# Kernel tuning notes

Hardware: AMD Instinct MI355X
Metric: run time of the kernel (lower is better)

The kernel has to match this reference:

```python
import jax, jax.numpy as jnp
import numpy as np

B = 2048      # batch (number of event graphs)
NU = 128      # nodes in 'upstream' star graph per sample
ND = 128      # nodes in 'downstream' star graph per sample
FEAT = 10     # raw feature columns; fp[:, :7] used, column -3 (=7) is split flag
IN_DIM = 7    # state_dim + 1 + 2
HID = 64      # hidden1
TAU = 22      # tau_num
ALPHA = 0.2


def star_adj(n):
    # prepare_eg: edges[0,:]=1, symmetrized, diagonal zeroed -> star graph around node 0
    idx = jnp.arange(n)
    return (((idx[:, None] == 0) | (idx[None, :] == 0)) & (idx[:, None] != idx[None, :])).astype(jnp.float32)


def gat(h, W, a, adj, concat):
    # pyGAT GraphAttentionLayer (dropout=0): h [B,n,f], W [f,d], a [2d,1]
    d = W.shape[1]
    Wh = jnp.einsum('bnf,fd->bnd', h, W)                      # [B,n,d]
    e = Wh @ a[:d] + jnp.swapaxes(Wh @ a[d:], 1, 2)           # [B,n,n]
    e = jax.nn.leaky_relu(e, ALPHA)
    e = jnp.where(adj > 0, e, -9e15)
    att = jax.nn.softmax(e, axis=-1)
    hp = jnp.einsum('bnm,bmd->bnd', att, Wh)                  # [B,n,d]
    return jax.nn.elu(hp) if concat else hp


def setup_inputs() -> dict:
    key = jax.random.key(0)
    ks = jax.random.split(key, 12)
    fp = jax.random.normal(ks[0], (B, NU + ND, FEAT), dtype=jnp.float32)
    # column -3: first NU rows negative (u side), last ND rows positive (d side)
    fp = fp.at[:, :NU, FEAT - 3].set(-1.0)
    fp = fp.at[:, NU:, FEAT - 3].set(1.0)
    s = 0.1
    return {
        'fp': fp,
        'u_att_W': jax.random.normal(ks[1], (IN_DIM, HID), jnp.float32) * s,
        'u_att_a': jax.random.normal(ks[2], (2 * HID, 1), jnp.float32) * s,
        'u_out_W': jax.random.normal(ks[3], (HID, HID), jnp.float32) * s,
        'u_out_a': jax.random.normal(ks[4], (2 * HID, 1), jnp.float32) * s,
        'd_att_W': jax.random.normal(ks[5], (IN_DIM, HID), jnp.float32) * s,
        'd_att_a': jax.random.normal(ks[6], (2 * HID, 1), jnp.float32) * s,
        'd_out_W': jax.random.normal(ks[7], (HID, HID), jnp.float32) * s,
        'd_out_a': jax.random.normal(ks[8], (2 * HID, 1), jnp.float32) * s,
        'fc2_W': jax.random.normal(ks[9], (HID, TAU), jnp.float32) * s,
        'fc2_b': jax.random.normal(ks[10], (TAU,), jnp.float32) * s,
    }


def reference(fp, u_att_W, u_att_a, u_out_W, u_out_a,
              d_att_W, d_att_a, d_out_W, d_out_a, fc2_W, fc2_b):
    # static split by the sign of column -3 (fp is constructed so the first NU
    # rows have flag<=0 and the last ND rows have flag>=0, matching prepare_eg)
    u_x = fp[:, :NU, :IN_DIM]   # [B,NU,7]
    d_x = fp[:, NU:, :IN_DIM]   # [B,ND,7]
    u_adj = star_adj(NU)
    d_adj = star_adj(ND)
    # u_egat: 1 attention head (concat->elu) then out layer (no elu), sum over nodes
    u_h = gat(gat(u_x, u_att_W, u_att_a, u_adj, True), u_out_W, u_out_a, u_adj, False)
    u_g = jnp.sum(u_h, axis=1)  # [B,HID]
    d_h = gat(gat(d_x, d_att_W, d_att_a, d_adj, True), d_out_W, d_out_a, d_adj, False)
    d_g = jnp.sum(d_h, axis=1)  # [B,HID]
    a = jax.nn.relu((u_g + d_g) @ fc2_W + fc2_b)  # [B,TAU]
    # torch.sort result is discarded; forward returns W.clamp(0, 10)
    return jnp.clip(a, 0.0, 10.0)
```

## Files before the change

### kernel.cpp

```cpp
#include <hip/hip_runtime.h>
#include <math.h>

#define NB     2048
#define FEAT   10
#define IN_DIM 7
#define HID    64
#define TAU    22
#define ALPHA  0.2f

__global__ __launch_bounds__(256) void gat_star_one(
    const float* __restrict__ fp,
    const float* __restrict__ uW1, const float* __restrict__ uA1,
    const float* __restrict__ uW2,
    const float* __restrict__ dW1, const float* __restrict__ dA1,
    const float* __restrict__ dW2,
    const float* __restrict__ fcW, const float* __restrict__ fcB,
    float* __restrict__ out)
{
    __shared__ float vv[2][2][HID];
    __shared__ float pt[2][2][HID];

    const int tid  = threadIdx.x;
    const int wave = tid >> 6;
    const int lane = tid & 63;
    const int it   = wave >> 1;
    const int half = wave & 1;
    const int item = blockIdx.x * 2 + it;

    const float* xbase = fp + (size_t)item * 256 * FEAT + half * 128 * FEAT;
    const float* pAp = xbase + lane * FEAT;
    const float* pBp = pAp + 64 * FEAT;
    const float2 a0 = *(const float2*)(pAp + 0);
    const float2 a1 = *(const float2*)(pAp + 2);
    const float2 a2 = *(const float2*)(pAp + 4);
    const float  a6 = pAp[6];
    const float2 b0 = *(const float2*)(pBp + 0);
    const float2 b1 = *(const float2*)(pBp + 2);
    const float2 b2 = *(const float2*)(pBp + 4);
    const float  b6 = pBp[6];

    const float* W1 = half ? dW1 : uW1;
    const float* A1 = half ? dA1 : uA1;
    float w1c[IN_DIM];
    #pragma unroll
    for (int f = 0; f < IN_DIM; ++f) w1c[f] = W1[f * HID + lane];
    const float alo = A1[lane];
    const float ahi = A1[HID + lane];

    float sv1[IN_DIM], sv2[IN_DIM];
    #pragma unroll
    for (int f = 0; f < IN_DIM; ++f) {
        float p1 = w1c[f] * alo;
        float p2 = w1c[f] * ahi;
        #pragma unroll
        for (int o = 32; o; o >>= 1) {
            p1 += __shfl_xor(p1, o);
            p2 += __shfl_xor(p2, o);
        }
        sv1[f] = p1; sv2[f] = p2;
    }

    float xA[IN_DIM], xB[IN_DIM];
    xA[0] = a0.x; xA[1] = a0.y; xA[2] = a1.x; xA[3] = a1.y;
    xA[4] = a2.x; xA[5] = a2.y; xA[6] = a6;
    xB[0] = b0.x; xB[1] = b0.y; xB[2] = b1.x; xB[3] = b1.y;
    xB[4] = b2.x; xB[5] = b2.y; xB[6] = b6;

    float x0[IN_DIM];
    #pragma unroll
    for (int f = 0; f < IN_DIM; ++f) x0[f] = __shfl(xA[f], 0);

    float s1 = 0.f, sA = 0.f, sB = 0.f;
    #pragma unroll
    for (int f = 0; f < IN_DIM; ++f) {
        s1 = fmaf(x0[f], sv1[f], s1);
        sA = fmaf(xA[f], sv2[f], sA);
        sB = fmaf(xB[f], sv2[f], sB);
    }
    float eA = s1 + sA; eA = (eA >= 0.f) ? eA : ALPHA * eA;
    float eB = s1 + sB; eB = (eB >= 0.f) ? eB : ALPHA * eB;

    const float qA = (lane == 0) ? 0.f : __expf(eA);
    const float qB = __expf(eB);
    float c[8];
    #pragma unroll
    for (int f = 0; f < IN_DIM; ++f) c[f] = fmaf(qA, xA[f], qB * xB[f]);
    c[7] = qA + qB;
    #pragma unroll
    for (int o = 32; o; o >>= 1) {
        #pragma unroll
        for (int j = 0; j < 8; ++j) c[j] += __shfl_xor(c[j], o);
    }
    const float inv = 1.0f / c[7];

    float h0 = 0.f, h1 = 0.f;
    #pragma unroll
    for (int f = 0; f < IN_DIM; ++f) {
        h0 = fmaf(c[f],  w1c[f], h0);
        h1 = fmaf(x0[f], w1c[f], h1);
    }
    h0 *= inv;
    h0 = (h0 > 0.f) ? h0 : (__expf(h0) - 1.f);
    h1 = (h1 > 0.f) ? h1 : (__expf(h1) - 1.f);
    vv[it][half][lane] = h1 + 127.f * h0;
    __syncthreads();

    {
        const float* W2 = half ? dW2 : uW2;
        const float* v  = vv[it][half];
        float s = 0.f;
        #pragma unroll 16
        for (int k = 0; k < HID; ++k) s = fmaf(v[k], W2[k * HID + lane], s);
        pt[it][half][lane] = s;
    }
    __syncthreads();

    if (half == 0) {
        const float* p0 = pt[it][0];
        const float* p1 = pt[it][1];
        int t = lane & 31; if (t > TAU - 1) t = TAU - 1;
        const int jb = (lane >> 5) << 5;
        float s = 0.f;
        #pragma unroll 8
        for (int jj = 0; jj < 32; ++jj) {
            const int j = jb + jj;
            s = fmaf(p0[j] + p1[j], fcW[j * TAU + t], s);
        }
        s += __shfl_xor(s, 32);
        if (lane < TAU) {
            s += fcB[lane];
            s = fminf(fmaxf(s, 0.f), 10.f);
            out[(size_t)item * TAU + lane] = s;
        }
    }
}

extern "C" void kernel_launch(void* const* d_in, const int* in_sizes, int n_in,
                              void* d_out, int out_size, void* d_ws, size_t ws_size,
                              hipStream_t stream) {
    const float* fp  = (const float*)d_in[0];
    const float* uW1 = (const float*)d_in[1];
    const float* uA1 = (const float*)d_in[2];
    const float* uW2 = (const float*)d_in[3];
    const float* dW1 = (const float*)d_in[5];
    const float* dA1 = (const float*)d_in[6];
    const float* dW2 = (const float*)d_in[7];
    const float* fcW = (const float*)d_in[9];
    const float* fcB = (const float*)d_in[10];
    float* out = (float*)d_out;

    gat_star_one<<<NB / 2, 256, 0, stream>>>(fp, uW1, uA1, uW2,
                                             dW1, dA1, dW2, fcW, fcB, out);
}
```

Baseline: 14.99 us.

## Use DPP wave reductions, per-wave fc2 partials, and wave barriers instead of block syncs

Replaces the shuffle-based butterfly reductions with DPP row/bank operations plus a readlane. The 14 attention-vector dot products are now computed per lane into LDS instead of by cross-lane reductions. Node 0's features are read directly from memory rather than broadcast by shuffle. Each wave computes its own partial fc2 product and only one block-wide sync remains before the final combine, with multiple accumulators added to break FMA dependency chains. The aim is to cut cross-lane latency and block synchronisation, at the cost of relying on DPP patterns being correct for a full 64-lane sum.

```diff
diff --git a/kernel.cpp b/kernel.cpp
--- a/kernel.cpp
+++ b/kernel.cpp
@@ -8,6 +8,22 @@
 #define TAU    22
 #define ALPHA  0.2f
 
+template <int CTRL>
+__device__ __forceinline__ float dpp_mv(float x) {
+    return __int_as_float(__builtin_amdgcn_update_dpp(
+        0, __float_as_int(x), CTRL, 0xf, 0xf, true));
+}
+
+__device__ __forceinline__ float wave_sum64(float v) {
+    v += dpp_mv<0xB1>(v);
+    v += dpp_mv<0x4E>(v);
+    v += dpp_mv<0x141>(v);
+    v += dpp_mv<0x140>(v);
+    v += dpp_mv<0x142>(v);
+    v += dpp_mv<0x143>(v);
+    return __int_as_float(__builtin_amdgcn_readlane(__float_as_int(v), 63));
+}
+
 __global__ __launch_bounds__(256) void gat_star_one(
     const float* __restrict__ fp,
     const float* __restrict__ uW1, const float* __restrict__ uA1,
@@ -17,8 +33,10 @@
     const float* __restrict__ fcW, const float* __restrict__ fcB,
     float* __restrict__ out)
 {
-    __shared__ float vv[2][2][HID];
-    __shared__ float pt[2][2][HID];
+    __shared__ float svs[4][16];
+    __shared__ float vvs[4][HID];
+    __shared__ float pts[4][HID];
+    __shared__ float rrs[4][TAU];
 
     const int tid  = threadIdx.x;
     const int wave = tid >> 6;
@@ -38,37 +56,47 @@
     const float2 b1 = *(const float2*)(pBp + 2);
     const float2 b2 = *(const float2*)(pBp + 4);
     const float  b6 = pBp[6];
+    const float4 x03 = *(const float4*)xbase;
+    const float2 x45 = *(const float2*)(xbase + 4);
+    const float  x6  = xbase[6];
 
     const float* W1 = half ? dW1 : uW1;
     const float* A1 = half ? dA1 : uA1;
     float w1c[IN_DIM];
     #pragma unroll
     for (int f = 0; f < IN_DIM; ++f) w1c[f] = W1[f * HID + lane];
-    const float alo = A1[lane];
-    const float ahi = A1[HID + lane];
 
-    float sv1[IN_DIM], sv2[IN_DIM];
-    #pragma unroll
-    for (int f = 0; f < IN_DIM; ++f) {
-        float p1 = w1c[f] * alo;
-        float p2 = w1c[f] * ahi;
+    if (lane < 14) {
+        const int sp = (lane >= IN_DIM) ? 1 : 0;
+        const int f  = lane - sp * IN_DIM;
+        const float* wr = W1 + f * HID;
+        const float* av = A1 + sp * HID;
+        float s0 = 0.f, s1 = 0.f, s2 = 0.f, s3 = 0.f;
         #pragma unroll
-        for (int o = 32; o; o >>= 1) {
-            p1 += __shfl_xor(p1, o);
-            p2 += __shfl_xor(p2, o);
+        for (int k = 0; k < HID; k += 4) {
+            s0 = fmaf(wr[k + 0], av[k + 0], s0);
+            s1 = fmaf(wr[k + 1], av[k + 1], s1);
+            s2 = fmaf(wr[k + 2], av[k + 2], s2);
+            s3 = fmaf(wr[k + 3], av[k + 3], s3);
         }
-        sv1[f] = p1; sv2[f] = p2;
+        svs[wave][sp * 8 + f] = (s0 + s1) + (s2 + s3);
     }
+    __builtin_amdgcn_wave_barrier();
 
-    float xA[IN_DIM], xB[IN_DIM];
+    float x0[IN_DIM], xA[IN_DIM], xB[IN_DIM];
+    x0[0] = x03.x; x0[1] = x03.y; x0[2] = x03.z; x0[3] = x03.w;
+    x0[4] = x45.x; x0[5] = x45.y; x0[6] = x6;
     xA[0] = a0.x; xA[1] = a0.y; xA[2] = a1.x; xA[3] = a1.y;
     xA[4] = a2.x; xA[5] = a2.y; xA[6] = a6;
     xB[0] = b0.x; xB[1] = b0.y; xB[2] = b1.x; xB[3] = b1.y;
     xB[4] = b2.x; xB[5] = b2.y; xB[6] = b6;
 
-    float x0[IN_DIM];
+    float sv1[IN_DIM], sv2[IN_DIM];
     #pragma unroll
-    for (int f = 0; f < IN_DIM; ++f) x0[f] = __shfl(xA[f], 0);
+    for (int f = 0; f < IN_DIM; ++f) {
+        sv1[f] = svs[wave][f];
+        sv2[f] = svs[wave][8 + f];
+    }
 
     float s1 = 0.f, sA = 0.f, sB = 0.f;
     #pragma unroll
@@ -84,13 +112,9 @@
     const float qB = __expf(eB);
     float c[8];
     #pragma unroll
-    for (int f = 0; f < IN_DIM; ++f) c[f] = fmaf(qA, xA[f], qB * xB[f]);
-    c[7] = qA + qB;
-    #pragma unroll
-    for (int o = 32; o; o >>= 1) {
-        #pragma unroll
-        for (int j = 0; j < 8; ++j) c[j] += __shfl_xor(c[j], o);
-    }
+    for (int f = 0; f < IN_DIM; ++f)
+        c[f] = wave_sum64(fmaf(qA, xA[f], qB * xB[f]));
+    c[7] = wave_sum64(qA + qB);
     const float inv = 1.0f / c[7];
 
     float h0 = 0.f, h1 = 0.f;
@@ -102,36 +126,44 @@
     h0 *= inv;
     h0 = (h0 > 0.f) ? h0 : (__expf(h0) - 1.f);
     h1 = (h1 > 0.f) ? h1 : (__expf(h1) - 1.f);
-    vv[it][half][lane] = h1 + 127.f * h0;
-    __syncthreads();
+    vvs[wave][lane] = h1 + 127.f * h0;
+    __builtin_amdgcn_wave_barrier();
 
     {
         const float* W2 = half ? dW2 : uW2;
-        const float* v  = vv[it][half];
-        float s = 0.f;
-        #pragma unroll 16
-        for (int k = 0; k < HID; ++k) s = fmaf(v[k], W2[k * HID + lane], s);
-        pt[it][half][lane] = s;
+        const float* v  = vvs[wave];
+        float t0 = 0.f, t1 = 0.f, t2 = 0.f, t3 = 0.f;
+        #pragma unroll
+        for (int k = 0; k < HID; k += 4) {
+            t0 = fmaf(v[k + 0], W2[(k + 0) * HID + lane], t0);
+            t1 = fmaf(v[k + 1], W2[(k + 1) * HID + lane], t1);
+            t2 = fmaf(v[k + 2], W2[(k + 2) * HID + lane], t2);
+            t3 = fmaf(v[k + 3], W2[(k + 3) * HID + lane], t3);
+        }
+        pts[wave][lane] = (t0 + t1) + (t2 + t3);
+    }
+    __builtin_amdgcn_wave_barrier();
+
+    {
+        const float* p = pts[wave];
+        int t = lane & 31; if (t > TAU - 1) t = TAU - 1;
+        const int jb = lane & 32;
+        float s0 = 0.f, s1_ = 0.f;
+        #pragma unroll
+        for (int jj = 0; jj < 32; jj += 2) {
+            s0  = fmaf(p[jb + jj],     fcW[(jb + jj)     * TAU + t], s0);
+            s1_ = fmaf(p[jb + jj + 1], fcW[(jb + jj + 1) * TAU + t], s1_);
+        }
+        float s = s0 + s1_;
+        s += __shfl_xor(s, 32);
+        if (lane < TAU) rrs[wave][lane] = s;
     }
     __syncthreads();
 
-    if (half == 0) {
-        const float* p0 = pt[it][0];
-        const float* p1 = pt[it][1];
-        int t = lane & 31; if (t > TAU - 1) t = TAU - 1;
-        const int jb = (lane >> 5) << 5;
-        float s = 0.f;
-        #pragma unroll 8
-        for (int jj = 0; jj < 32; ++jj) {
-            const int j = jb + jj;
-            s = fmaf(p0[j] + p1[j], fcW[j * TAU + t], s);
-        }
-        s += __shfl_xor(s, 32);
-        if (lane < TAU) {
-            s += fcB[lane];
-            s = fminf(fmaxf(s, 0.f), 10.f);
-            out[(size_t)item * TAU + lane] = s;
-        }
+    if (half == 0 && lane < TAU) {
+        float s = rrs[wave][lane] + rrs[wave + 1][lane] + fcB[lane];
+        s = fminf(fmaxf(s, 0.f), 10.f);
+        out[(size_t)item * TAU + lane] = s;
     }
 }
 
```

New measurement: 16.09 us. 1.07x slower.
